# Optimization experiments

Hardware: AMD Instinct MI355X
Metric: run time of the kernel (lower is better)

Reference implementation:

```python
import jax, jax.numpy as jnp
import numpy as np

EPS = 1e-8  # torch.nn.CosineSimilarity default eps


def setup_inputs() -> dict:
    key = jax.random.key(0)
    k1, k2, k3 = jax.random.split(key, 3)
    B, D = 4096, 768
    x = jax.random.normal(k1, (B, D), dtype=jnp.float32)
    fc_w = jax.random.normal(k2, (2, 1), dtype=jnp.float32) * (1.0)  # Linear(1,2) weight
    fc_b = jax.random.normal(k3, (2,), dtype=jnp.float32)
    return {"x": x, "fc_w": fc_w, "fc_b": fc_b}


def reference(x, fc_w, fc_b):
    # Pairwise cosine similarity via normalize-then-GEMM.
    # torch CosineSimilarity: dot(a,b) / (max(||a||, eps) * max(||b||, eps))
    norms = jnp.maximum(jnp.linalg.norm(x, axis=-1, keepdims=True), EPS)  # [B,1]
    xn = x / norms                                                        # [B,D]
    sim = jnp.einsum('id,jd->ij', xn, xn)                                 # [B,B]
    # fc: Linear(1,2) on sim.unsqueeze(-1): out[...,k] = sim * w[k,0] + b[k]
    out = sim[..., None] * fc_w[:, 0] + fc_b                              # [B,B,2]
    return out
```

## Files before the change

kernel.cpp:

```cpp
#include <hip/hip_runtime.h>
#include <hip/hip_bf16.h>

typedef int i32x4 __attribute__((ext_vector_type(4)));
typedef int i32x8 __attribute__((ext_vector_type(8)));
typedef float f32x4 __attribute__((ext_vector_type(4)));

#define KD 768
#define BDIM 4096
#define NSTRIP 16
#define E8M0_1_8TH 124
#define BLDS 24576

#define GLOAD_LDS16(gptr, lptr)                                             \
    __builtin_amdgcn_global_load_lds(                                       \
        (const __attribute__((address_space(1))) unsigned int*)(gptr),      \
        (__attribute__((address_space(3))) unsigned int*)(lptr), 16, 0, 0)

#define FBAR() asm volatile("s_barrier" ::: "memory")
#define SCHED_FENCE() __builtin_amdgcn_sched_barrier(0)

__device__ inline unsigned char f32_to_e4m3(float f) {
    int p = __builtin_amdgcn_cvt_pk_fp8_f32(f, f, 0, false);
    return (unsigned char)(p & 0xFF);
}

__global__ __launch_bounds__(256) void normalize_rows_fp8(
    const float* __restrict__ x, unsigned char* __restrict__ xn)
{
    const int row = blockIdx.x;
    const int t = threadIdx.x;
    const float* xr = x + (long)row * KD;

    float v[3];
    float ss = 0.f;
#pragma unroll
    for (int i = 0; i < 3; ++i) {
        v[i] = xr[t + 256 * i];
        ss += v[i] * v[i];
    }
#pragma unroll
    for (int off = 32; off > 0; off >>= 1) ss += __shfl_down(ss, off);
    __shared__ float wss[4];
    const int lane = t & 63, wv = t >> 6;
    if (lane == 0) wss[wv] = ss;
    __syncthreads();
    const float tot = wss[0] + wss[1] + wss[2] + wss[3];
    const float inv = 8.0f / fmaxf(sqrtf(tot), 1e-8f);
#pragma unroll
    for (int i = 0; i < 3; ++i)
        xn[(long)row * KD + t + 256 * i] = f32_to_e4m3(v[i] * inv);
}

__global__ __launch_bounds__(512) void sim_gemm_stream(
    const unsigned char* __restrict__ Xn,
    const float* __restrict__ fcw, const float* __restrict__ fcb,
    float* __restrict__ out)
{
    __shared__ __align__(16) unsigned char Bb[2][BLDS];

    const int tid = threadIdx.x;
    const int wv  = tid >> 6;
    const int ln  = tid & 63;
    const int wm  = wv >> 1;
    const int wn  = wv & 1;
    const int fr  = ln & 15;
    const int q   = ln >> 4;

    const int jc = blockIdx.x;
    const int bi = blockIdx.y;
    const long Arow0 = (long)bi * 128;
    const long Bcol0 = (long)jc * 512;

    int scol[3], skoff[3];
#pragma unroll
    for (int i = 0; i < 3; ++i) {
        const int d = i * 8192 + tid * 16;
        scol[i]  = (d >> 6) & 31;
        skoff[i] = ((d >> 12) << 7) + (((d >> 4) & 3) << 5) + (((d >> 11) & 1) << 4);
    }

#define ISSUE_B(s) do {                                                      \
        _Pragma("unroll")                                                    \
        for (int i_ = 0; i_ < 3; ++i_) {                                     \
            const unsigned char* g_ = Xn                                     \
                + (Bcol0 + (s) * 32 + scol[i_]) * (long)KD + skoff[i_];      \
            unsigned char* l_ = &Bb[(s) & 1][0] + i_ * 8192 + wv * 1024;     \
            GLOAD_LDS16(g_, l_);                                             \
        }                                                                    \
    } while (0)

    i32x8 aF[2][6];
    {
        const unsigned char* pa0 = Xn + (Arow0 + wm * 32 + fr) * (long)KD + q * 32;
        const unsigned char* pa1 = pa0 + 16 * (long)KD;
#pragma unroll
        for (int kk = 0; kk < 6; ++kk) {
            i32x4 lo0 = *(const i32x4*)(pa0 + kk * 128);
            i32x4 hi0 = *(const i32x4*)(pa0 + kk * 128 + 16);
            aF[0][kk] = __builtin_shufflevector(lo0, hi0, 0, 1, 2, 3, 4, 5, 6, 7);
            i32x4 lo1 = *(const i32x4*)(pa1 + kk * 128);
            i32x4 hi1 = *(const i32x4*)(pa1 + kk * 128 + 16);
            aF[1][kk] = __builtin_shufflevector(lo1, hi1, 0, 1, 2, 3, 4, 5, 6, 7);
        }
    }

    const float w0 = fcw[0], w1 = fcw[1];
    const float c0 = fcb[0], c1 = fcb[1];

    ISSUE_B(0);
    asm volatile("s_waitcnt vmcnt(0)" ::: "memory");
    FBAR();

    const int colbase = (int)Bcol0 + wn * 16 + fr;
    const long rowb   = Arow0 + wm * 32 + q * 4;

    for (int s = 0; s < NSTRIP; ++s) {
        const int bb = s & 1;

        if (s + 1 < NSTRIP) ISSUE_B(s + 1);
        SCHED_FENCE();

        f32x4 acc[2] = {};
#pragma unroll
        for (int kk = 0; kk < 6; ++kk) {
            const int bo = kk * 4096 + (wn * 16 + fr) * 64 + q * 16;
            i32x4 lo = *(const i32x4*)&Bb[bb][bo];
            i32x4 hi = *(const i32x4*)&Bb[bb][bo + 2048];
            i32x8 bv = __builtin_shufflevector(lo, hi, 0, 1, 2, 3, 4, 5, 6, 7);
            __builtin_amdgcn_s_setprio(1);
            acc[0] = __builtin_amdgcn_mfma_scale_f32_16x16x128_f8f6f4(
                aF[0][kk], bv, acc[0], 0, 0, 0, E8M0_1_8TH, 0, E8M0_1_8TH);
            acc[1] = __builtin_amdgcn_mfma_scale_f32_16x16x128_f8f6f4(
                aF[1][kk], bv, acc[1], 0, 0, 0, E8M0_1_8TH, 0, E8M0_1_8TH);
            __builtin_amdgcn_s_setprio(0);
        }

        const int col = colbase + s * 32;
#pragma unroll
        for (int mf = 0; mf < 2; ++mf)
#pragma unroll
            for (int rr = 0; rr < 4; ++rr) {
                const long row = rowb + mf * 16 + rr;
                const float sv = acc[mf][rr];
                *(float2*)&out[(row * BDIM + col) * 2] =
                    make_float2(fmaf(sv, w0, c0), fmaf(sv, w1, c1));
            }

        if (s + 1 < NSTRIP) {
            asm volatile("s_waitcnt vmcnt(8)" ::: "memory");
            FBAR();
        }
    }

#undef ISSUE_B
}

extern "C" void kernel_launch(void* const* d_in, const int* in_sizes, int n_in,
                              void* d_out, int out_size, void* d_ws, size_t ws_size,
                              hipStream_t stream) {
    const float* x   = (const float*)d_in[0];
    const float* fcw = (const float*)d_in[1];
    const float* fcb = (const float*)d_in[2];
    float* out = (float*)d_out;

    unsigned char* xn = (unsigned char*)d_ws;

    normalize_rows_fp8<<<BDIM, 256, 0, stream>>>(x, xn);

    dim3 grid(8, 32);
    sim_gemm_stream<<<grid, 512, 0, stream>>>(xn, fcw, fcb, out);
}
```

Baseline: 41.33 us.

## Widen B strips to 64 columns and triple-buffer LDS with prefetch distance two

Each strip now covers 64 output columns, so a wave computes two N fragments per K step and reuses each A fragment across both. There are 8 strips instead of 16. The LDS B buffer grows to three 48 KB stages, and loads are issued two strips ahead, with the waitcnt values adjusted to match. The aim is to cut per-strip barrier and wait overhead and hide global-to-LDS latency better, at the cost of about 144 KB of LDS per block, so one block fits per CU. The kernel is likely bound by the 128 MB output write, which limits how much this can help.

```diff
diff --git a/kernel.cpp b/kernel.cpp
--- a/kernel.cpp
+++ b/kernel.cpp
@@ -7,9 +7,9 @@
 
 #define KD 768
 #define BDIM 4096
-#define NSTRIP 16
+#define NSTRIP 8
 #define E8M0_1_8TH 124
-#define BLDS 24576
+#define BLDS 49152
 
 #define GLOAD_LDS16(gptr, lptr)                                             \
     __builtin_amdgcn_global_load_lds(                                       \
@@ -51,12 +51,12 @@
         xn[(long)row * KD + t + 256 * i] = f32_to_e4m3(v[i] * inv);
 }
 
-__global__ __launch_bounds__(512) void sim_gemm_stream(
+__global__ __launch_bounds__(512, 2) void sim_gemm_stream(
     const unsigned char* __restrict__ Xn,
     const float* __restrict__ fcw, const float* __restrict__ fcb,
     float* __restrict__ out)
 {
-    __shared__ __align__(16) unsigned char Bb[2][BLDS];
+    __shared__ __align__(16) unsigned char Bb[3][BLDS];
 
     const int tid = threadIdx.x;
     const int wv  = tid >> 6;
@@ -71,20 +71,20 @@
     const long Arow0 = (long)bi * 128;
     const long Bcol0 = (long)jc * 512;
 
-    int scol[3], skoff[3];
+    int scol[6], skoff[6];
 #pragma unroll
-    for (int i = 0; i < 3; ++i) {
+    for (int i = 0; i < 6; ++i) {
         const int d = i * 8192 + tid * 16;
-        scol[i]  = (d >> 6) & 31;
-        skoff[i] = ((d >> 12) << 7) + (((d >> 4) & 3) << 5) + (((d >> 11) & 1) << 4);
+        scol[i]  = (d >> 6) & 63;
+        skoff[i] = ((d >> 13) << 7) + (((d >> 4) & 3) << 5) + (((d >> 12) & 1) << 4);
     }
 
 #define ISSUE_B(s) do {                                                      \
         _Pragma("unroll")                                                    \
-        for (int i_ = 0; i_ < 3; ++i_) {                                     \
+        for (int i_ = 0; i_ < 6; ++i_) {                                     \
             const unsigned char* g_ = Xn                                     \
-                + (Bcol0 + (s) * 32 + scol[i_]) * (long)KD + skoff[i_];      \
-            unsigned char* l_ = &Bb[(s) & 1][0] + i_ * 8192 + wv * 1024;     \
+                + (Bcol0 + (s) * 64 + scol[i_]) * (long)KD + skoff[i_];      \
+            unsigned char* l_ = &Bb[(s) % 3][0] + i_ * 8192 + wv * 1024;     \
             GLOAD_LDS16(g_, l_);                                             \
         }                                                                    \
     } while (0)
@@ -108,46 +108,52 @@
     const float c0 = fcb[0], c1 = fcb[1];
 
     ISSUE_B(0);
-    asm volatile("s_waitcnt vmcnt(0)" ::: "memory");
+    ISSUE_B(1);
+    asm volatile("s_waitcnt vmcnt(6)" ::: "memory");
     FBAR();
 
-    const int colbase = (int)Bcol0 + wn * 16 + fr;
-    const long rowb   = Arow0 + wm * 32 + q * 4;
+    const int colb0 = (int)Bcol0 + wn * 32 + fr;
+    const long rowb = Arow0 + wm * 32 + q * 4;
 
     for (int s = 0; s < NSTRIP; ++s) {
-        const int bb = s & 1;
+        const int bb = s % 3;
 
-        if (s + 1 < NSTRIP) ISSUE_B(s + 1);
+        if (s + 2 < NSTRIP) ISSUE_B(s + 2);
         SCHED_FENCE();
 
-        f32x4 acc[2] = {};
+        f32x4 acc[2][2] = {};
 #pragma unroll
         for (int kk = 0; kk < 6; ++kk) {
-            const int bo = kk * 4096 + (wn * 16 + fr) * 64 + q * 16;
-            i32x4 lo = *(const i32x4*)&Bb[bb][bo];
-            i32x4 hi = *(const i32x4*)&Bb[bb][bo + 2048];
-            i32x8 bv = __builtin_shufflevector(lo, hi, 0, 1, 2, 3, 4, 5, 6, 7);
-            __builtin_amdgcn_s_setprio(1);
-            acc[0] = __builtin_amdgcn_mfma_scale_f32_16x16x128_f8f6f4(
-                aF[0][kk], bv, acc[0], 0, 0, 0, E8M0_1_8TH, 0, E8M0_1_8TH);
-            acc[1] = __builtin_amdgcn_mfma_scale_f32_16x16x128_f8f6f4(
-                aF[1][kk], bv, acc[1], 0, 0, 0, E8M0_1_8TH, 0, E8M0_1_8TH);
-            __builtin_amdgcn_s_setprio(0);
+#pragma unroll
+            for (int nf = 0; nf < 2; ++nf) {
+                const int bo = kk * 8192 + (wn * 32 + nf * 16 + fr) * 64 + q * 16;
+                i32x4 lo = *(const i32x4*)&Bb[bb][bo];
+                i32x4 hi = *(const i32x4*)&Bb[bb][bo + 4096];
+                i32x8 bv = __builtin_shufflevector(lo, hi, 0, 1, 2, 3, 4, 5, 6, 7);
+                __builtin_amdgcn_s_setprio(1);
+                acc[0][nf] = __builtin_amdgcn_mfma_scale_f32_16x16x128_f8f6f4(
+                    aF[0][kk], bv, acc[0][nf], 0, 0, 0, E8M0_1_8TH, 0, E8M0_1_8TH);
+                acc[1][nf] = __builtin_amdgcn_mfma_scale_f32_16x16x128_f8f6f4(
+                    aF[1][kk], bv, acc[1][nf], 0, 0, 0, E8M0_1_8TH, 0, E8M0_1_8TH);
+                __builtin_amdgcn_s_setprio(0);
+            }
         }
 
-        const int col = colbase + s * 32;
+        const int col = colb0 + s * 64;
 #pragma unroll
         for (int mf = 0; mf < 2; ++mf)
 #pragma unroll
-            for (int rr = 0; rr < 4; ++rr) {
-                const long row = rowb + mf * 16 + rr;
-                const float sv = acc[mf][rr];
-                *(float2*)&out[(row * BDIM + col) * 2] =
-                    make_float2(fmaf(sv, w0, c0), fmaf(sv, w1, c1));
-            }
+            for (int nf = 0; nf < 2; ++nf)
+#pragma unroll
+                for (int rr = 0; rr < 4; ++rr) {
+                    const long row = rowb + mf * 16 + rr;
+                    const float sv = acc[mf][nf][rr];
+                    *(float2*)&out[(row * BDIM + col + nf * 16) * 2] =
+                        make_float2(fmaf(sv, w0, c0), fmaf(sv, w1, c1));
+                }
 
         if (s + 1 < NSTRIP) {
-            asm volatile("s_waitcnt vmcnt(8)" ::: "memory");
+            asm volatile("s_waitcnt vmcnt(16)" ::: "memory");
             FBAR();
         }
     }
```

Result: slower. 42.41 us (+2.6%).
